# Kernel tuning notes

Hardware: AMD Instinct MI355X
Metric: run time of the kernel (lower is better)

## Reference

```python
import jax, jax.numpy as jnp
import numpy as np

LMAX = 4
DSH = (LMAX + 1) ** 2          # 25 spherical-harmonic coefficients
C = 32                          # channels per degree l
N = 10000                       # nodes
E = 160000                      # edges
FC = 64                         # fc_len_in (radial/edge scalar feature dim)

# flattened (l,m) index = l^2 + l + m
IDX0 = np.array([l * l + l for l in range(LMAX + 1)])               # m = 0 coeffs
POS = {m: np.array([l * l + l + m for l in range(m, LMAX + 1)]) for m in range(1, LMAX + 1)}
NEG = {m: np.array([l * l + l - m for l in range(m, LMAX + 1)]) for m in range(1, LMAX + 1)}
L_OF_IDX = np.concatenate([np.full(2 * l + 1, l) for l in range(LMAX + 1)])  # degree of each coeff


def setup_inputs() -> dict:
    key = jax.random.key(0)
    ks = jax.random.split(key, 20)
    inp = {
        "x": jax.random.normal(ks[0], (N, DSH, C), jnp.float32),
        "wigner": jax.random.normal(ks[1], (E, DSH, DSH), jnp.float32) * 0.2,
        "edge_fc": jax.random.normal(ks[2], (E, FC), jnp.float32),
        "edge_src": jax.random.randint(ks[3], (E,), 0, N),
        "edge_dst": jax.random.randint(ks[4], (E,), 0, N),
    }
    # per-m SO(2) block weights
    d0 = (LMAX + 1) * C
    inp["w0"] = jax.random.normal(ks[5], (d0, d0), jnp.float32) / np.sqrt(d0)
    k = 6
    for m in range(1, LMAX + 1):
        dm = (LMAX + 1 - m) * C
        inp[f"w{m}r"] = jax.random.normal(ks[k], (dm, dm), jnp.float32) / np.sqrt(dm); k += 1
        inp[f"w{m}i"] = jax.random.normal(ks[k], (dm, dm), jnp.float32) / np.sqrt(dm); k += 1
    # radial/cfconv network producing per-(degree, channel) scales
    inp["fc_w"] = jax.random.normal(ks[k], (FC, (LMAX + 1) * C), jnp.float32) / np.sqrt(FC)
    inp["fc_b"] = jnp.zeros(((LMAX + 1) * C,), jnp.float32)
    return inp


def reference(x, wigner, edge_fc, edge_src, edge_dst,
              w0, w1r, w1i, w2r, w2i, w3r, w3i, w4r, w4i, fc_w, fc_b):
    Wr = {1: w1r, 2: w2r, 3: w3r, 4: w4r}
    Wi = {1: w1i, 2: w2i, 3: w3i, 4: w4i}
    # gather node features to edges and rotate into edge-aligned frame
    xe = x[edge_src]                                   # [E, 25, C]
    xr = jnp.einsum('eij,ejc->eic', wigner, xe)        # [E, 25, C]
    Ee = xr.shape[0]
    y = jnp.zeros_like(xr)
    # m = 0 block: real linear over stacked-l channels
    x0 = xr[:, IDX0, :].reshape(Ee, -1)                # [E, 5*C]
    y = y.at[:, IDX0, :].set((x0 @ w0).reshape(Ee, LMAX + 1, C))
    # m > 0 blocks: SO(2) complex-style mixing
    for m in range(1, LMAX + 1):
        pos, neg = POS[m], NEG[m]
        Lm = len(pos)
        xp = xr[:, pos, :].reshape(Ee, -1)             # [E, Lm*C]
        xn = xr[:, neg, :].reshape(Ee, -1)
        yp = xp @ Wr[m] - xn @ Wi[m]
        yn = xp @ Wi[m] + xn @ Wr[m]
        y = y.at[:, pos, :].set(yp.reshape(Ee, Lm, C))
        y = y.at[:, neg, :].set(yn.reshape(Ee, Lm, C))
    # cfconv: per-edge radial scaling, one scalar per (degree, channel)
    scale = jax.nn.silu(edge_fc @ fc_w + fc_b).reshape(Ee, LMAX + 1, C)
    y = y * scale[:, L_OF_IDX, :]
    # rotate back (Wigner D is orthogonal -> transpose is inverse)
    yb = jnp.einsum('eji,ejc->eic', wigner, y)
    # scatter-aggregate messages to destination nodes
    return jax.ops.segment_sum(yb, edge_dst, num_segments=N)
```

## Files before the change

kernel.cpp:

```cpp
#include <hip/hip_runtime.h>

typedef __attribute__((ext_vector_type(8))) short short8;
typedef __attribute__((ext_vector_type(4))) short short4v;
typedef __attribute__((ext_vector_type(4))) float f32x4;

#define MFMA16(a,b,c) __builtin_amdgcn_mfma_f32_16x16x32_bf16((a),(b),(c),0,0,0)

__device__ __align__(16) short g_wt[117760];
__device__ __align__(16) short g_wtf[148480];
__device__ __align__(16) short g_fcwt[10240];

struct K2Tab {
  int   fbase[50];
  int   pboff[50][8];
  short acoeff[50][8];
  short len[50];
  short dm[50];
  short ut[50];
  short ocoeff[50];
  short lsc[50];
  short co16[50];
  short pu[290];
  short pk[290];
};

constexpr K2Tab make_k2tab() {
  K2Tab T{};
  const int P[5][5]  = {{0,2,6,12,20},{3,7,13,21,0},{8,14,22,0,0},{15,23,0,0,0},{24,0,0,0,0}};
  const int Ng[5][5] = {{0,0,0,0,0},{1,5,11,19,0},{4,10,18,0,0},{9,17,0,0,0},{16,0,0,0,0}};
  const int WR[5]  = {0, 25600, 74752, 102400, 114688};
  const int WI[5]  = {0, 41984, 83968, 106496, 115712};
  const int NWI[5] = {0, 58368, 93184, 110592, 116736};
  const int ms[9]  = {1,1,2,2,0,3,3,4,4};
  const int hs[9]  = {0,1,0,1,0,0,1,0,1};
  const int ntc[9] = {8,8,6,6,10,4,4,2,2};
  int u = 0, fb = 0, np = 0;
  for (int g = 0; g < 9; ++g) {
    const int m = ms[g], h = hs[g];
    const int dm = (m == 0) ? 160 : (5 - m) * 32;
    const int lm = (m == 0) ? 5 : (5 - m);
    const int len = (m == 0) ? 5 : 2 * lm;
    const int b1 = (m == 0) ? 0 : ((h == 0) ? WR[m] : WI[m]);
    const int b2 = (m == 0) ? 0 : ((h == 0) ? NWI[m] : WR[m]);
    for (int tt = 0; tt < ntc[g]; ++tt, ++u) {
      T.dm[u] = (short)dm; T.len[u] = (short)len; T.ut[u] = (short)tt;
      const int lo = tt >> 1;
      T.ocoeff[u] = (short)((m == 0) ? P[0][lo] : ((h == 0) ? P[m][lo] : Ng[m][lo]));
      T.lsc[u] = (short)(m + lo);
      T.co16[u] = (short)((tt & 1) * 16);
      T.fbase[u] = fb;
      for (int k = 0; k < len; ++k) {
        int bb, ac;
        if (m == 0)      { bb = k * 32;            ac = P[0][k]; }
        else if (k < lm) { bb = b1 + k * 32;       ac = P[m][k]; }
        else             { bb = b2 + (k - lm) * 32; ac = Ng[m][k - lm]; }
        T.pboff[u][k] = bb; T.acoeff[u][k] = (short)ac;
        T.pu[np] = (short)u; T.pk[np] = (short)k; ++np;
      }
      fb += len * 512;
    }
  }
  return T;
}
__constant__ K2Tab c_kt = make_k2tab();

__device__ __forceinline__ short f2bf(float f) {
  unsigned u = __float_as_uint(f);
  u += 0x7FFFu + ((u >> 16) & 1u);
  return (short)(u >> 16);
}

__global__ void prep_weights(const float* __restrict__ w0,
    const float* __restrict__ w1r, const float* __restrict__ w1i,
    const float* __restrict__ w2r, const float* __restrict__ w2i,
    const float* __restrict__ w3r, const float* __restrict__ w3i,
    const float* __restrict__ w4r, const float* __restrict__ w4i,
    const float* __restrict__ fcw) {
  int idx = blockIdx.x * 256 + threadIdx.x;
  if (idx >= 128000) return;
  if (idx >= 117760) {
    int local = idx - 117760;
    int n = local >> 6, k = local & 63;
    g_fcwt[local] = f2bf(fcw[k * 160 + n]);
    return;
  }
  int off, dm; const float* src; bool neg = false;
  if (idx < 25600)       { off = 0;      dm = 160; src = w0;  }
  else if (idx < 41984)  { off = 25600;  dm = 128; src = w1r; }
  else if (idx < 58368)  { off = 41984;  dm = 128; src = w1i; }
  else if (idx < 74752)  { off = 58368;  dm = 128; src = w1i; neg = true; }
  else if (idx < 83968)  { off = 74752;  dm = 96;  src = w2r; }
  else if (idx < 93184)  { off = 83968;  dm = 96;  src = w2i; }
  else if (idx < 102400) { off = 93184;  dm = 96;  src = w2i; neg = true; }
  else if (idx < 106496) { off = 102400; dm = 64;  src = w3r; }
  else if (idx < 110592) { off = 106496; dm = 64;  src = w3i; }
  else if (idx < 114688) { off = 110592; dm = 64;  src = w3i; neg = true; }
  else if (idx < 115712) { off = 114688; dm = 32;  src = w4r; }
  else if (idx < 116736) { off = 115712; dm = 32;  src = w4i; }
  else                   { off = 116736; dm = 32;  src = w4i; neg = true; }
  int local = idx - off;
  int n = local / dm, k = local - n * dm;
  float v = src[k * dm + n];
  g_wt[idx] = f2bf(neg ? -v : v);
}

__global__ void prep_frags() {
  int i = blockIdx.x * 256 + threadIdx.x;
  if (i >= 290 * 512) return;
  int p = i >> 9;
  int w = i & 511;
  int lane = w >> 3, j = w & 7;
  int l15 = lane & 15, lg = lane >> 4;
  int u = c_kt.pu[p], k = c_kt.pk[p];
  int col = (int)c_kt.ut[u] * 16 + l15;
  g_wtf[i] = g_wt[c_kt.pboff[u][k] + col * (int)c_kt.dm[u] + lg * 8 + j];
}

__global__ void hist_kernel(const int* __restrict__ edst, int* __restrict__ cnt, int E) {
  int i = blockIdx.x * 256 + threadIdx.x;
  if (i < E) atomicAdd(&cnt[edst[i]], 1);
}

__global__ __launch_bounds__(1024) void scan_kernel(
    const int* __restrict__ cnt, int* __restrict__ cursor, int N) {
  __shared__ int s[1024];
  const int t = threadIdx.x;
  int v[10]; int sum = 0;
  #pragma unroll
  for (int k = 0; k < 10; ++k) {
    int i = t * 10 + k;
    v[k] = (i < N) ? cnt[i] : 0;
    sum += v[k];
  }
  s[t] = sum;
  __syncthreads();
  for (int d = 1; d < 1024; d <<= 1) {
    int add = (t >= d) ? s[t - d] : 0;
    __syncthreads();
    s[t] += add;
    __syncthreads();
  }
  int prefix = s[t] - sum;
  #pragma unroll
  for (int k = 0; k < 10; ++k) {
    int i = t * 10 + k;
    if (i < N) cursor[i] = prefix;
    prefix += v[k];
  }
}

__global__ void scatter_kernel(const int* __restrict__ edst, int* __restrict__ cursor,
                               int* __restrict__ order, int E) {
  int i = blockIdx.x * 256 + threadIdx.x;
  if (i < E) {
    int p = atomicAdd(&cursor[edst[i]], 1);
    order[p] = i;
  }
}

__global__ __launch_bounds__(512, 6) void k12_fused(
    const float* __restrict__ x, const float* __restrict__ wig,
    const float* __restrict__ efc, const int* __restrict__ esrc,
    const int* __restrict__ order, const float* __restrict__ fcb,
    short* __restrict__ y, int E)
{
  __shared__ __align__(16) short s_buf[16 * 1304];
  __shared__ _Float16 s_sc[16 * 168];
  __shared__ int s_meta[32];

  const int tid = threadIdx.x;
  const int lane = tid & 63;
  const int wid = tid >> 6;
  const int l15 = lane & 15;
  const int lg  = lane >> 4;
  const int koff = lg * 8;
  const int e0  = blockIdx.x * 16;

  for (int o = tid; o < 10432; o += 512) ((int*)s_buf)[o] = 0;
  if (tid < 16) {
    int idx = min(e0 + tid, E - 1);
    int og = order[idx];
    s_meta[tid] = og;
    s_meta[16 + tid] = esrc[og];
  }
  __syncthreads();

  for (int o = tid; o < 12800; o += 512) {
    int e = o / 800, q = o - e * 800;
    s_buf[e * 1304 + (q & 31) * 40 + (q >> 5)] = f2bf(x[(size_t)s_meta[16 + e] * 800 + q]);
  }
  {
    const int ge = s_meta[l15];
    const float* ep = efc + (size_t)ge * 64;
    float4 fa = *(const float4*)(ep + lg * 8);
    float4 fb = *(const float4*)(ep + lg * 8 + 4);
    float4 fc = *(const float4*)(ep + 32 + lg * 8);
    float4 fd = *(const float4*)(ep + 32 + lg * 8 + 4);
    short8 af0, af1;
    af0[0]=f2bf(fa.x); af0[1]=f2bf(fa.y); af0[2]=f2bf(fa.z); af0[3]=f2bf(fa.w);
    af0[4]=f2bf(fb.x); af0[5]=f2bf(fb.y); af0[6]=f2bf(fb.z); af0[7]=f2bf(fb.w);
    af1[0]=f2bf(fc.x); af1[1]=f2bf(fc.y); af1[2]=f2bf(fc.z); af1[3]=f2bf(fc.w);
    af1[4]=f2bf(fd.x); af1[5]=f2bf(fd.y); af1[6]=f2bf(fd.z); af1[7]=f2bf(fd.w);
    for (int nt = wid; nt < 10; nt += 8) {
      const int f = nt * 16 + l15;
      const short* bp = g_fcwt + f * 64 + lg * 8;
      short8 b0 = *(const short8*)(bp);
      short8 b1 = *(const short8*)(bp + 32);
      f32x4 acc = {0.f, 0.f, 0.f, 0.f};
      acc = MFMA16(af0, b0, acc);
      acc = MFMA16(af1, b1, acc);
      float bias = fcb[f];
      #pragma unroll
      for (int r = 0; r < 4; ++r) {
        float vv = acc[r] + bias;
        s_sc[(lg * 4 + r) * 168 + (f >> 5) * 33 + (f & 31)] =
            (_Float16)(vv / (1.f + __expf(-vv)));
      }
    }
  }
  __syncthreads();

  f32x4 d00[2], d01[2], d10[2], d11[2];
  #pragma unroll
  for (int i = 0; i < 2; ++i) {
    const int e = wid * 2 + i;
    const short* xeb = s_buf + e * 1304;
    const float* wp = wig + (size_t)s_meta[e] * 625;
    short8 a0 = *(const short8*)(xeb + l15 * 40 + koff);
    short8 a1 = *(const short8*)(xeb + (16 + l15) * 40 + koff);
    short8 b0, b1;
    const int r1 = min(16 + l15, 24);
    #pragma unroll
    for (int j = 0; j < 8; ++j) {
      const int k = koff + j;
      const int kc = min(k, 24);
      const short v0 = f2bf(wp[l15 * 25 + kc]);
      const short v1 = f2bf(wp[r1 * 25 + kc]);
      b0[j] = (k < 25) ? v0 : (short)0;
      b1[j] = (k < 25) ? v1 : (short)0;
    }
    f32x4 t00 = {0.f,0.f,0.f,0.f}, t01 = {0.f,0.f,0.f,0.f};
    f32x4 t10 = {0.f,0.f,0.f,0.f}, t11 = {0.f,0.f,0.f,0.f};
    t00 = MFMA16(a0, b0, t00);
    t01 = MFMA16(a0, b1, t01);
    t10 = MFMA16(a1, b0, t10);
    t11 = MFMA16(a1, b1, t11);
    d00[i] = t00; d01[i] = t01; d10[i] = t10; d11[i] = t11;
  }
  __syncthreads();

  #pragma unroll
  for (int i = 0; i < 2; ++i) {
    const int e = wid * 2 + i;
    short* xp = s_buf + e * 1304;
    short4v v;
    v[0]=f2bf(d00[i][0]); v[1]=f2bf(d00[i][1]); v[2]=f2bf(d00[i][2]); v[3]=f2bf(d00[i][3]);
    *(short4v*)(xp + l15 * 32 + lg * 4) = v;
    v[0]=f2bf(d10[i][0]); v[1]=f2bf(d10[i][1]); v[2]=f2bf(d10[i][2]); v[3]=f2bf(d10[i][3]);
    *(short4v*)(xp + l15 * 32 + 16 + lg * 4) = v;
    if (l15 < 9) {
      v[0]=f2bf(d01[i][0]); v[1]=f2bf(d01[i][1]); v[2]=f2bf(d01[i][2]); v[3]=f2bf(d01[i][3]);
      *(short4v*)(xp + (16 + l15) * 32 + lg * 4) = v;
      v[0]=f2bf(d11[i][0]); v[1]=f2bf(d11[i][1]); v[2]=f2bf(d11[i][2]); v[3]=f2bf(d11[i][3]);
      *(short4v*)(xp + (16 + l15) * 32 + 16 + lg * 4) = v;
    }
  }
  __syncthreads();

  for (int u = wid; u < 50; u += 8) {
    const int len = c_kt.len[u];
    const short* Bp = g_wtf + c_kt.fbase[u] + lane * 8;
    short8 B[8];
    #pragma unroll 8
    for (int k = 0; k < 8; ++k)
      if (k < len) B[k] = *(const short8*)(Bp + (k << 9));
    const int co = c_kt.co16[u] + l15;
    const int oc = c_kt.ocoeff[u];
    const int ls = c_kt.lsc[u];
    const short* xl = s_buf + l15 * 1304 + koff;
    f32x4 acc0 = {0.f,0.f,0.f,0.f}, acc1 = {0.f,0.f,0.f,0.f};
    #pragma unroll 8
    for (int k = 0; k < 8; ++k) {
      if (k < len) {
        short8 a = *(const short8*)(xl + (int)c_kt.acoeff[u][k] * 32);
        if (k & 1) acc1 = MFMA16(a, B[k], acc1);
        else       acc0 = MFMA16(a, B[k], acc0);
      }
    }
    f32x4 acc = acc0 + acc1;
    #pragma unroll
    for (int r = 0; r < 4; ++r) {
      const int el = lg * 4 + r;
      const int slot = e0 + el;
      if (slot < E) {
        float sc = (float)s_sc[el * 168 + ls * 33 + co];
        y[(size_t)slot * 800 + oc * 32 + co] = f2bf(acc[r] * sc);
      }
    }
  }
}

__global__ __launch_bounds__(256, 5) void k3_back(
    const short* __restrict__ y, const float* __restrict__ wig,
    const int* __restrict__ edst, const int* __restrict__ order,
    const int* __restrict__ cnt, float* __restrict__ out, int E)
{
  __shared__ __align__(16) char sumem[27136];
  __shared__ int s_meta[64];
  short* s_y  = (short*)sumem;
  float* yb_s = (float*)sumem;

  const int tid = threadIdx.x;
  const int lane = tid & 63;
  const int wid = tid >> 6;
  const int l15 = lane & 15;
  const int lg  = lane >> 4;
  const int e0  = blockIdx.x * 8;

  for (int o = tid; o < 5216; o += 256) ((int*)sumem)[o] = 0;
  if (tid < 8) {
    int idx = e0 + tid;
    bool v = idx < E;
    int og = order[v ? idx : 0];
    s_meta[tid] = og;
    s_meta[16 + tid] = v ? edst[og] : -1;
  }
  __syncthreads();

  if (wid == 0) {
    int dj = (lane < 8) ? s_meta[16 + lane] : -1;
    bool valid = (lane < 8) && (dj >= 0);
    bool is_start = valid && (lane == 0 || dj != s_meta[16 + lane - 1]);
    unsigned long long vm = __ballot(valid);
    unsigned long long sm = __ballot(is_start);
    int nv = __popcll(vm);
    int ng = __popcll(sm);
    if (lane == 0) s_meta[24] = ng;
    if ((int)lane < ng) {
      int s = -1, c = -1;
      for (int b = 0; b < 8; ++b) { if ((sm >> b) & 1) { ++c; if (c == (int)lane) { s = b; break; } } }
      int e_ = nv;
      for (int b = s + 1; b < 8; ++b) if ((sm >> b) & 1) { e_ = b; break; }
      int d = s_meta[16 + s];
      s_meta[25 + lane] = d;
      s_meta[33 + lane] = s;
      s_meta[41 + lane] = e_;
      s_meta[49 + lane] = ((e_ - s) == cnt[d]) ? 1 : 0;
    }
  }
  for (int o = tid; o < 800; o += 256) {
    int e = o / 100, r = o - e * 100;
    int slot = min(e0 + e, E - 1);
    int q = r * 8;
    *(short8*)(s_y + e * 1304 + (q >> 5) * 40 + (q & 31)) =
        *(const short8*)(y + (size_t)slot * 800 + q);
  }
  __syncthreads();

  f32x4 r00[2], r01[2], r10[2], r11[2];
  #pragma unroll
  for (int i = 0; i < 2; ++i) {
    const int e = wid * 2 + i;
    const short* yb = s_y + e * 1304 + lg * 8 * 40;
    const float* wp = wig + (size_t)s_meta[e] * 625;
    short8 a0, a1, b0, b1;
    const int c2 = min(16 + l15, 24);
    #pragma unroll 8
    for (int j = 0; j < 8; ++j) {
      a0[j] = yb[j * 40 + l15];
      a1[j] = yb[j * 40 + 16 + l15];
      const int k = lg * 8 + j;
      const int kc = min(k, 24);
      const short v0 = f2bf(wp[kc * 25 + l15]);
      const short v1 = f2bf(wp[kc * 25 + c2]);
      b0[j] = (k < 25) ? v0 : (short)0;
      b1[j] = (k < 25) ? v1 : (short)0;
    }
    f32x4 d00 = {0.f,0.f,0.f,0.f}, d01 = {0.f,0.f,0.f,0.f};
    f32x4 d10 = {0.f,0.f,0.f,0.f}, d11 = {0.f,0.f,0.f,0.f};
    d00 = MFMA16(a0, b0, d00);
    d01 = MFMA16(a0, b1, d01);
    d10 = MFMA16(a1, b0, d10);
    d11 = MFMA16(a1, b1, d11);
    r00[i] = d00; r01[i] = d01; r10[i] = d10; r11[i] = d11;
  }
  __syncthreads();

  #pragma unroll
  for (int i = 0; i < 2; ++i) {
    const int e = wid * 2 + i;
    float* yb = yb_s + e * 840;
    #pragma unroll 4
    for (int r = 0; r < 4; ++r) {
      yb[l15 * 33 + lg * 4 + r]      = r00[i][r];
      yb[l15 * 33 + 16 + lg * 4 + r] = r10[i][r];
    }
    if (l15 < 9) {
      #pragma unroll 4
      for (int r = 0; r < 4; ++r) {
        yb[(16 + l15) * 33 + lg * 4 + r]      = r01[i][r];
        yb[(16 + l15) * 33 + 16 + lg * 4 + r] = r11[i][r];
      }
    }
  }
  __syncthreads();

  const int ng = s_meta[24];
  for (int o = tid; o < 800; o += 256) {
    const int yoff = (o >> 5) * 33 + (o & 31);
    for (int g = 0; g < ng; ++g) {
      float sum = 0.f;
      const int gs = s_meta[33 + g], ge = s_meta[41 + g];
      for (int e = gs; e < ge; ++e) sum += yb_s[e * 840 + yoff];
      float* ad = out + (size_t)s_meta[25 + g] * 800 + o;
      if (s_meta[49 + g]) *ad = sum;
      else atomicAdd(ad, sum);
    }
  }
}

extern "C" void kernel_launch(void* const* d_in, const int* in_sizes, int n_in,
                              void* d_out, int out_size, void* d_ws, size_t ws_size,
                              hipStream_t stream) {
  const float* x    = (const float*)d_in[0];
  const float* wigp = (const float*)d_in[1];
  const float* efc  = (const float*)d_in[2];
  const int*   esrc = (const int*)d_in[3];
  const int*   edst = (const int*)d_in[4];
  const float* w0   = (const float*)d_in[5];
  const float* w1r  = (const float*)d_in[6];
  const float* w1i  = (const float*)d_in[7];
  const float* w2r  = (const float*)d_in[8];
  const float* w2i  = (const float*)d_in[9];
  const float* w3r  = (const float*)d_in[10];
  const float* w3i  = (const float*)d_in[11];
  const float* w4r  = (const float*)d_in[12];
  const float* w4i  = (const float*)d_in[13];
  const float* fcw  = (const float*)d_in[14];
  const float* fcb  = (const float*)d_in[15];
  float* out = (float*)d_out;
  const int E = in_sizes[3];
  const int N = out_size / 800;

  int* cnt    = (int*)d_ws;
  int* cursor = cnt + N;
  int* order  = cnt + 2 * N;
  size_t y_off = (((size_t)(2 * N + E) * 4) + 255) & ~(size_t)255;
  short* yb = (short*)((char*)d_ws + y_off);

  prep_weights<<<(128000 + 255) / 256, 256, 0, stream>>>(
      w0, w1r, w1i, w2r, w2i, w3r, w3i, w4r, w4i, fcw);
  prep_frags<<<(290 * 512 + 255) / 256, 256, 0, stream>>>();

  hipMemsetAsync(d_out, 0, (size_t)out_size * sizeof(float), stream);
  hipMemsetAsync(cnt, 0, (size_t)N * sizeof(int), stream);

  hist_kernel<<<(E + 255) / 256, 256, 0, stream>>>(edst, cnt, E);
  scan_kernel<<<1, 1024, 0, stream>>>(cnt, cursor, N);
  scatter_kernel<<<(E + 255) / 256, 256, 0, stream>>>(edst, cursor, order, E);

  k12_fused<<<(E + 15) / 16, 512, 0, stream>>>(
      x, wigp, efc, esrc, order, fcb, yb, E);
  k3_back<<<(E + 7) / 8, 256, 0, stream>>>(yb, wigp, edst, order, cnt, out, E);
}
```

Before: 783.3 us.

## Process 32 edges per block in fused rotate+SO2 kernel to reuse weight fragments

Doubles the edges per k12_fused block from 16 to 32, so each B-fragment of the SO(2) block weights loaded from global memory is reused across two 16-edge M-tiles. The gathered x layout changes from a transposed, padded stride to a row-major stride, with only the padding region zeroed. The rotation A-fragments are now built from scalar LDS reads. Each edge's rotation result is written back immediately, which removes one barrier. This uses dynamic shared memory of about 78KB and lowers the launch-bounds occupancy target from 6 to 4, trading occupancy and more LDS bank traffic for less weight-load bandwidth.

Result: no change. 770.3 us (-1.7%).

```diff
diff --git a/kernel.cpp b/kernel.cpp
--- a/kernel.cpp
+++ b/kernel.cpp
@@ -158,15 +158,19 @@
   }
 }
 
-__global__ __launch_bounds__(512, 6) void k12_fused(
+#define ESTRIDE 1048
+#define SMEM_K12 78080
+
+__global__ __launch_bounds__(512, 4) void k12_fused(
     const float* __restrict__ x, const float* __restrict__ wig,
     const float* __restrict__ efc, const int* __restrict__ esrc,
     const int* __restrict__ order, const float* __restrict__ fcb,
     short* __restrict__ y, int E)
 {
-  __shared__ __align__(16) short s_buf[16 * 1304];
-  __shared__ _Float16 s_sc[16 * 168];
-  __shared__ int s_meta[32];
+  extern __shared__ char smem[];
+  short*     s_buf  = (short*)smem;
+  _Float16*  s_sc   = (_Float16*)(smem + 67072);
+  int*       s_meta = (int*)(smem + 77824);
 
   const int tid = threadIdx.x;
   const int lane = tid & 63;
@@ -174,23 +178,27 @@
   const int l15 = lane & 15;
   const int lg  = lane >> 4;
   const int koff = lg * 8;
-  const int e0  = blockIdx.x * 16;
-
-  for (int o = tid; o < 10432; o += 512) ((int*)s_buf)[o] = 0;
-  if (tid < 16) {
+  const int e0  = blockIdx.x * 32;
+
+  for (int o = tid; o < 3584; o += 512) {
+    int e = o / 112, q = o - e * 112;
+    ((int*)s_buf)[e * 524 + 400 + q] = 0;
+  }
+  if (tid < 32) {
     int idx = min(e0 + tid, E - 1);
     int og = order[idx];
     s_meta[tid] = og;
-    s_meta[16 + tid] = esrc[og];
-  }
-  __syncthreads();
-
-  for (int o = tid; o < 12800; o += 512) {
+    s_meta[32 + tid] = esrc[og];
+  }
+  __syncthreads();
+
+  for (int o = tid; o < 25600; o += 512) {
     int e = o / 800, q = o - e * 800;
-    s_buf[e * 1304 + (q & 31) * 40 + (q >> 5)] = f2bf(x[(size_t)s_meta[16 + e] * 800 + q]);
+    s_buf[e * ESTRIDE + q] = f2bf(x[(size_t)s_meta[32 + e] * 800 + q]);
   }
   {
-    const int ge = s_meta[l15];
+    const int mt = wid >> 2;
+    const int ge = s_meta[mt * 16 + l15];
     const float* ep = efc + (size_t)ge * 64;
     float4 fa = *(const float4*)(ep + lg * 8);
     float4 fb = *(const float4*)(ep + lg * 8 + 4);
@@ -201,7 +209,7 @@
     af0[4]=f2bf(fb.x); af0[5]=f2bf(fb.y); af0[6]=f2bf(fb.z); af0[7]=f2bf(fb.w);
     af1[0]=f2bf(fc.x); af1[1]=f2bf(fc.y); af1[2]=f2bf(fc.z); af1[3]=f2bf(fc.w);
     af1[4]=f2bf(fd.x); af1[5]=f2bf(fd.y); af1[6]=f2bf(fd.z); af1[7]=f2bf(fd.w);
-    for (int nt = wid; nt < 10; nt += 8) {
+    for (int nt = (wid & 3); nt < 10; nt += 4) {
       const int f = nt * 16 + l15;
       const short* bp = g_fcwt + f * 64 + lg * 8;
       short8 b0 = *(const short8*)(bp);
@@ -213,21 +221,25 @@
       #pragma unroll
       for (int r = 0; r < 4; ++r) {
         float vv = acc[r] + bias;
-        s_sc[(lg * 4 + r) * 168 + (f >> 5) * 33 + (f & 31)] =
+        s_sc[(mt * 16 + lg * 4 + r) * 168 + (f >> 5) * 33 + (f & 31)] =
             (_Float16)(vv / (1.f + __expf(-vv)));
       }
     }
   }
   __syncthreads();
 
-  f32x4 d00[2], d01[2], d10[2], d11[2];
-  #pragma unroll
-  for (int i = 0; i < 2; ++i) {
-    const int e = wid * 2 + i;
-    const short* xeb = s_buf + e * 1304;
+  #pragma unroll 4
+  for (int i = 0; i < 4; ++i) {
+    const int e = wid * 4 + i;
+    short* eb = s_buf + e * ESTRIDE;
     const float* wp = wig + (size_t)s_meta[e] * 625;
-    short8 a0 = *(const short8*)(xeb + l15 * 40 + koff);
-    short8 a1 = *(const short8*)(xeb + (16 + l15) * 40 + koff);
+    short8 a0, a1;
+    #pragma unroll
+    for (int j = 0; j < 8; ++j) {
+      const int k = koff + j;
+      a0[j] = eb[k * 32 + l15];
+      a1[j] = eb[k * 32 + 16 + l15];
+    }
     short8 b0, b1;
     const int r1 = min(16 + l15, 24);
     #pragma unroll
@@ -239,30 +251,22 @@
       b0[j] = (k < 25) ? v0 : (short)0;
       b1[j] = (k < 25) ? v1 : (short)0;
     }
-    f32x4 t00 = {0.f,0.f,0.f,0.f}, t01 = {0.f,0.f,0.f,0.f};
-    f32x4 t10 = {0.f,0.f,0.f,0.f}, t11 = {0.f,0.f,0.f,0.f};
-    t00 = MFMA16(a0, b0, t00);
-    t01 = MFMA16(a0, b1, t01);
-    t10 = MFMA16(a1, b0, t10);
-    t11 = MFMA16(a1, b1, t11);
-    d00[i] = t00; d01[i] = t01; d10[i] = t10; d11[i] = t11;
-  }
-  __syncthreads();
-
-  #pragma unroll
-  for (int i = 0; i < 2; ++i) {
-    const int e = wid * 2 + i;
-    short* xp = s_buf + e * 1304;
+    f32x4 d00 = {0.f,0.f,0.f,0.f}, d01 = {0.f,0.f,0.f,0.f};
+    f32x4 d10 = {0.f,0.f,0.f,0.f}, d11 = {0.f,0.f,0.f,0.f};
+    d00 = MFMA16(a0, b0, d00);
+    d01 = MFMA16(a0, b1, d01);
+    d10 = MFMA16(a1, b0, d10);
+    d11 = MFMA16(a1, b1, d11);
     short4v v;
-    v[0]=f2bf(d00[i][0]); v[1]=f2bf(d00[i][1]); v[2]=f2bf(d00[i][2]); v[3]=f2bf(d00[i][3]);
-    *(short4v*)(xp + l15 * 32 + lg * 4) = v;
-    v[0]=f2bf(d10[i][0]); v[1]=f2bf(d10[i][1]); v[2]=f2bf(d10[i][2]); v[3]=f2bf(d10[i][3]);
-    *(short4v*)(xp + l15 * 32 + 16 + lg * 4) = v;
+    v[0]=f2bf(d00[0]); v[1]=f2bf(d00[1]); v[2]=f2bf(d00[2]); v[3]=f2bf(d00[3]);
+    *(short4v*)(eb + l15 * 32 + lg * 4) = v;
+    v[0]=f2bf(d10[0]); v[1]=f2bf(d10[1]); v[2]=f2bf(d10[2]); v[3]=f2bf(d10[3]);
+    *(short4v*)(eb + l15 * 32 + 16 + lg * 4) = v;
     if (l15 < 9) {
-      v[0]=f2bf(d01[i][0]); v[1]=f2bf(d01[i][1]); v[2]=f2bf(d01[i][2]); v[3]=f2bf(d01[i][3]);
-      *(short4v*)(xp + (16 + l15) * 32 + lg * 4) = v;
-      v[0]=f2bf(d11[i][0]); v[1]=f2bf(d11[i][1]); v[2]=f2bf(d11[i][2]); v[3]=f2bf(d11[i][3]);
-      *(short4v*)(xp + (16 + l15) * 32 + 16 + lg * 4) = v;
+      v[0]=f2bf(d01[0]); v[1]=f2bf(d01[1]); v[2]=f2bf(d01[2]); v[3]=f2bf(d01[3]);
+      *(short4v*)(eb + (16 + l15) * 32 + lg * 4) = v;
+      v[0]=f2bf(d11[0]); v[1]=f2bf(d11[1]); v[2]=f2bf(d11[2]); v[3]=f2bf(d11[3]);
+      *(short4v*)(eb + (16 + l15) * 32 + 16 + lg * 4) = v;
     }
   }
   __syncthreads();
@@ -277,24 +281,27 @@
     const int co = c_kt.co16[u] + l15;
     const int oc = c_kt.ocoeff[u];
     const int ls = c_kt.lsc[u];
-    const short* xl = s_buf + l15 * 1304 + koff;
-    f32x4 acc0 = {0.f,0.f,0.f,0.f}, acc1 = {0.f,0.f,0.f,0.f};
-    #pragma unroll 8
-    for (int k = 0; k < 8; ++k) {
-      if (k < len) {
-        short8 a = *(const short8*)(xl + (int)c_kt.acoeff[u][k] * 32);
-        if (k & 1) acc1 = MFMA16(a, B[k], acc1);
-        else       acc0 = MFMA16(a, B[k], acc0);
+    #pragma unroll 2
+    for (int mt = 0; mt < 2; ++mt) {
+      const short* xl = s_buf + (mt * 16 + l15) * ESTRIDE + koff;
+      f32x4 acc0 = {0.f,0.f,0.f,0.f}, acc1 = {0.f,0.f,0.f,0.f};
+      #pragma unroll 8
+      for (int k = 0; k < 8; ++k) {
+        if (k < len) {
+          short8 a = *(const short8*)(xl + (int)c_kt.acoeff[u][k] * 32);
+          if (k & 1) acc1 = MFMA16(a, B[k], acc1);
+          else       acc0 = MFMA16(a, B[k], acc0);
+        }
       }
-    }
-    f32x4 acc = acc0 + acc1;
-    #pragma unroll
-    for (int r = 0; r < 4; ++r) {
-      const int el = lg * 4 + r;
-      const int slot = e0 + el;
-      if (slot < E) {
-        float sc = (float)s_sc[el * 168 + ls * 33 + co];
-        y[(size_t)slot * 800 + oc * 32 + co] = f2bf(acc[r] * sc);
+      f32x4 acc = acc0 + acc1;
+      #pragma unroll
+      for (int r = 0; r < 4; ++r) {
+        const int el = mt * 16 + lg * 4 + r;
+        const int slot = e0 + el;
+        if (slot < E) {
+          float sc = (float)s_sc[el * 168 + ls * 33 + co];
+          y[(size_t)slot * 800 + oc * 32 + co] = f2bf(acc[r] * sc);
+        }
       }
     }
   }
@@ -448,6 +455,9 @@
   size_t y_off = (((size_t)(2 * N + E) * 4) + 255) & ~(size_t)255;
   short* yb = (short*)((char*)d_ws + y_off);
 
+  hipFuncSetAttribute((const void*)k12_fused,
+                      hipFuncAttributeMaxDynamicSharedMemorySize, SMEM_K12);
+
   prep_weights<<<(128000 + 255) / 256, 256, 0, stream>>>(
       w0, w1r, w1i, w2r, w2i, w3r, w3i, w4r, w4i, fcw);
   prep_frags<<<(290 * 512 + 255) / 256, 256, 0, stream>>>();
@@ -459,7 +469,7 @@
   scan_kernel<<<1, 1024, 0, stream>>>(cnt, cursor, N);
   scatter_kernel<<<(E + 255) / 256, 256, 0, stream>>>(edst, cursor, order, E);
 
-  k12_fused<<<(E + 15) / 16, 512, 0, stream>>>(
+  k12_fused<<<(E + 31) / 32, 512, SMEM_K12, stream>>>(
       x, wigp, efc, esrc, order, fcb, yb, E);
   k3_back<<<(E + 7) / 8, 256, 0, stream>>>(yb, wigp, edst, order, cnt, out, E);
 }
```
